# Kernel optimization log

Hardware: AMD Instinct MI355X
Metric: run time of the kernel (lower is better)

## Reference

```python
import jax, jax.numpy as jnp
import numpy as np
from jax import lax

SEQ, BATCH, IN, HID = 128, 512, 512, 512


def setup_inputs() -> dict:
    key = jax.random.key(0)
    k1, k2, k3 = jax.random.split(key, 3)
    # xavier_uniform over fan_in/fan_out of last two dims
    lim_ih = np.sqrt(6.0 / (IN + HID))
    lim_hh = np.sqrt(6.0 / (HID + HID))
    return {
        "inputs": jax.random.normal(k1, (SEQ, BATCH, IN), dtype=jnp.float32),
        "weight_ih": jax.random.uniform(k2, (8, IN, HID), jnp.float32, -lim_ih, lim_ih),
        "weight_hh": jax.random.uniform(k3, (8, HID, HID), jnp.float32, -lim_hh, lim_hh),
    }


def _cell(inp, state_c, state_m, weight_ih, weight_hh):
    # inp: [B, I]; states: [B, H]; weights: [8, I/H, H]
    s = jnp.einsum('bi,kih->kbh', inp, weight_ih) + jnp.einsum('bh,kho->kbo', state_m, weight_hh)
    l1_0 = jax.nn.sigmoid(s[0])
    l1_1 = jax.nn.relu(s[1])
    l1_2 = jax.nn.sigmoid(s[2])
    l1_3 = jax.nn.relu(s[3])
    l1_4 = jnp.tanh(s[4])
    l1_5 = jax.nn.sigmoid(s[5])
    l1_6 = jnp.tanh(s[6])
    l1_7 = jax.nn.sigmoid(s[7])
    l2_0 = jnp.tanh(l1_0 * l1_1)
    l2_1 = jnp.tanh(l1_2 + l1_3)
    l2_2 = jnp.tanh(l1_4 * l1_5)
    l2_3 = jax.nn.sigmoid(l1_6 + l1_7)
    l2_0_v2 = jnp.tanh(l2_0 + state_c)
    new_c = l2_0_v2 * l2_1
    l3_1 = jnp.tanh(l2_2 + l2_3)
    new_m = jnp.tanh(new_c * l3_1)
    return new_c, new_m


def reference(inputs, weight_ih, weight_hh):
    B = inputs.shape[1]
    H = weight_hh.shape[-1]
    init = (jnp.ones((B, H), inputs.dtype), jnp.ones((B, H), inputs.dtype))

    def step(carry, inp):
        c, m = carry
        c, m = _cell(inp, c, m, weight_ih, weight_hh)
        return (c, m), None

    (c, m), _ = lax.scan(step, init, inputs)
    return m
```

## Files before the change

### kernel.cpp

```cpp
#include <hip/hip_runtime.h>

#define SEQ  128
#define B_   512
#define IN_  512
#define HID_ 512
#define KTOT 1536
#define NTOT 4096
#define BM   64
#define BN   128
#define BK   64
#define NKT  (KTOT/BK)

typedef _Float16 f16;
typedef _Float16 f16x8 __attribute__((ext_vector_type(8)));
typedef _Float16 f16x4 __attribute__((ext_vector_type(4)));
typedef float    f32x4 __attribute__((ext_vector_type(4)));

#define OFF_BT  0u
#define OFF_X16 12582912u
#define OFF_C   79691776u
#define OFF_MH  80740352u
#define OFF_ML  81788928u

__device__ __forceinline__ void gll16(const void* g, void* l) {
  __builtin_amdgcn_global_load_lds(
      (const __attribute__((address_space(1))) unsigned int*)g,
      (__attribute__((address_space(3))) unsigned int*)l,
      16, 0, 0);
}

__device__ __forceinline__ float sigm_f(float x) {
  return __fdividef(1.f, 1.f + __expf(-x));
}
__device__ __forceinline__ float tanh_f(float x) {
  x = fminf(fmaxf(x, -15.f), 15.f);
  float u = __expf(2.f * x);
  return __fdividef(u - 1.f, u + 1.f);
}


__global__ void build_bt(const float* __restrict__ wih,
                         const float* __restrict__ whh,
                         f16* __restrict__ bt) {
  int n  = blockIdx.x;
  int hl = n & 15, k = (n >> 4) & 7, ht = n >> 7;
  int h  = ht * 16 + hl;
  const float* pih = wih + (size_t)k * IN_ * HID_ + h;
  const float* phh = whh + (size_t)k * HID_ * HID_ + h;
  f16* dst = bt + (size_t)n * KTOT;
  for (int r = threadIdx.x; r < 512; r += 256) {
    float a = pih[(size_t)r * HID_];
    float b = phh[(size_t)r * HID_];
    dst[r]        = (f16)a;
    dst[512 + r]  = (f16)b;
    dst[1024 + r] = (f16)b;
  }
}

__global__ void cvt_x(const float4* __restrict__ x, f16x4* __restrict__ y, int nvec) {
  int i = blockIdx.x * blockDim.x + threadIdx.x;
  int stride = gridDim.x * blockDim.x;
  for (; i < nvec; i += stride) {
    float4 v = x[i];
    f16x4 o = { (f16)v.x, (f16)v.y, (f16)v.z, (f16)v.w };
    y[i] = o;
  }
}

__global__ void init_state(float* __restrict__ c, f16* __restrict__ mh, f16* __restrict__ ml) {
  int i = blockIdx.x * blockDim.x + threadIdx.x;
  c[i]  = 1.f;
  mh[i] = (f16)1.f;
  ml[i] = (f16)0.f;
}

__global__ __launch_bounds__(256)
void nas_step(const f16* __restrict__ xt,
              const f16* __restrict__ bt,
              const f16* __restrict__ mh_in,
              const f16* __restrict__ ml_in,
              f16* __restrict__ mh_out,
              f16* __restrict__ ml_out,
              float* __restrict__ cst,
              float* __restrict__ out,
              int last) {
  __shared__ char lds[49152];
  char* Abase = lds;
  char* Bbase = lds + 16384;

  const int tid  = threadIdx.x;
  const int lane = tid & 63;
  const int wid  = tid >> 6;
  const int nt   = blockIdx.x;
  const int mt   = blockIdx.y;

  const f16* asrc[3] = { xt, mh_in, ml_in };

  auto stageA = [&](int buf, int kt) {
    const f16* src = asrc[kt >> 3];
    int kofs = (kt & 7) * BK;
#pragma unroll
    for (int p = 0; p < 2; ++p) {
      int u = p * 256 + tid;
      int r = u >> 3;
      int c16 = (u & 7) ^ (r & 7);
      gll16(src + ((size_t)(mt * BM + r) << 9) + kofs + c16 * 8,
            Abase + buf * 8192 + (p * 256 + wid * 64) * 16);
    }
  };
  auto stageB = [&](int buf, int kt) {
    int kg = kt * BK;
#pragma unroll
    for (int p = 0; p < 4; ++p) {
      int u = p * 256 + tid;
      int r = u >> 3;
      int c16 = (u & 7) ^ (r & 7);
      gll16(bt + (size_t)(nt * BN + r) * KTOT + kg + c16 * 8,
            Bbase + buf * 16384 + (p * 256 + wid * 64) * 16);
    }
  };

  f32x4 acc[8];
#pragma unroll
  for (int i = 0; i < 8; ++i) acc[i] = (f32x4){0.f, 0.f, 0.f, 0.f};

  stageA(0, 0); stageB(0, 0);
  __syncthreads();

  for (int kt = 0; kt < NKT; ++kt) {
    int cur = kt & 1;
    if (kt + 1 < NKT) { stageA(cur ^ 1, kt + 1); stageB(cur ^ 1, kt + 1); }
    const char* At = Abase + cur * 8192;
    const char* Bt = Bbase + cur * 16384;
#pragma unroll
    for (int kk = 0; kk < 2; ++kk) {
      int cb = (kk * 32 + ((lane >> 4) << 3)) * 2;
      int ra = wid * 16 + (lane & 15);
      f16x8 a = *(const f16x8*)(At + ra * 128 + (cb ^ ((ra & 7) << 4)));
#pragma unroll
      for (int ni = 0; ni < 8; ++ni) {
        int rb = ni * 16 + (lane & 15);
        f16x8 b = *(const f16x8*)(Bt + rb * 128 + (cb ^ ((rb & 7) << 4)));
        acc[ni] = __builtin_amdgcn_mfma_f32_16x16x32_f16(a, b, acc[ni], 0, 0, 0);
      }
    }
    __syncthreads();
  }

  const int h = nt * 16 + (lane & 15);
  const int rb4 = (lane >> 4) << 2;
#pragma unroll
  for (int q = 0; q < 4; ++q) {
    int b = mt * 64 + wid * 16 + rb4 + q;
    size_t idx = ((size_t)b << 9) + h;
    float l10 = sigm_f(acc[0][q]);
    float l11 = fmaxf(acc[1][q], 0.f);
    float l12 = sigm_f(acc[2][q]);
    float l13 = fmaxf(acc[3][q], 0.f);
    float l14 = tanh_f(acc[4][q]);
    float l15 = sigm_f(acc[5][q]);
    float l16 = tanh_f(acc[6][q]);
    float l17 = sigm_f(acc[7][q]);
    float l20 = tanh_f(l10 * l11);
    float l21 = tanh_f(l12 + l13);
    float l22 = tanh_f(l14 * l15);
    float l23 = sigm_f(l16 + l17);
    float cn  = tanh_f(l20 + cst[idx]) * l21;
    float l31 = tanh_f(l22 + l23);
    float mn  = tanh_f(cn * l31);
    cst[idx] = cn;
    f16 mh = (f16)mn;
    mh_out[idx] = mh;
    ml_out[idx] = (f16)(mn - (float)mh);
    if (last) out[idx] = mn;
  }
}

extern "C" void kernel_launch(void* const* d_in, const int* in_sizes, int n_in,
                              void* d_out, int out_size, void* d_ws, size_t ws_size,
                              hipStream_t stream) {
  const float* inputs = (const float*)d_in[0];
  const float* wih    = (const float*)d_in[1];
  const float* whh    = (const float*)d_in[2];
  float* out = (float*)d_out;
  char* ws   = (char*)d_ws;

  f16*   BT  = (f16*)(ws + OFF_BT);
  f16*   X16 = (f16*)(ws + OFF_X16);
  float* C   = (float*)(ws + OFF_C);
  f16*   MH  = (f16*)(ws + OFF_MH);
  f16*   ML  = (f16*)(ws + OFF_ML);

  build_bt<<<NTOT, 256, 0, stream>>>(wih, whh, BT);
  cvt_x<<<2048, 256, 0, stream>>>((const float4*)inputs, (f16x4*)X16,
                                  SEQ * B_ * IN_ / 4);
  init_state<<<1024, 256, 0, stream>>>(C, MH, ML);

  for (int t = 0; t < SEQ; ++t) {
    int cur = t & 1;
    nas_step<<<dim3(32, 8), 256, 0, stream>>>(
        X16 + (size_t)t * B_ * IN_, BT,
        MH + (size_t)cur * (B_ * HID_), ML + (size_t)cur * (B_ * HID_),
        MH + (size_t)(cur ^ 1) * (B_ * HID_), ML + (size_t)(cur ^ 1) * (B_ * HID_),
        C, out, (t == SEQ - 1) ? 1 : 0);
  }
}
```

Before: 2.234 ms.

## Fuse all timesteps into a persistent cooperative kernel with a grid barrier

Replaces the 128 per-timestep launches with one persistent cooperative kernel of 256 blocks. Blocks synchronise through an atomic counter in global memory and keep the cell state c in registers. A 5-slot LDS pipeline prefetches the next timestep's x tiles and the weight tiles across the barrier. The weight matrix is stored with a single copy of W_hh that serves both the m-high and m-low halves, and the B fragments are reused between them. This removes per-launch overhead and the global round-trips for c. In exchange it relies on all blocks being co-resident and on hand-tuned vmcnt waits, which could deadlock or race if the counts are wrong.

```diff
diff --git a/kernel.cpp b/kernel.cpp
--- a/kernel.cpp
+++ b/kernel.cpp
@@ -2,31 +2,27 @@
 
 #define SEQ  128
 #define B_   512
-#define IN_  512
 #define HID_ 512
-#define KTOT 1536
-#define NTOT 4096
-#define BM   64
-#define BN   128
-#define BK   64
-#define NKT  (KTOT/BK)
+#define NKT  24
 
 typedef _Float16 f16;
 typedef _Float16 f16x8 __attribute__((ext_vector_type(8)));
-typedef _Float16 f16x4 __attribute__((ext_vector_type(4)));
 typedef float    f32x4 __attribute__((ext_vector_type(4)));
 
-#define OFF_BT  0u
-#define OFF_X16 12582912u
-#define OFF_C   79691776u
-#define OFF_MH  80740352u
-#define OFF_ML  81788928u
+#define OFF_BT   0u
+#define OFF_X16  8388608u
+#define OFF_MH   75497472u
+#define OFF_ML   76546048u
+#define OFF_C    77594624u
+#define OFF_BAR  78643200u
+
+#define SLOT  24576
+#define NSLOT 5
 
 __device__ __forceinline__ void gll16(const void* g, void* l) {
   __builtin_amdgcn_global_load_lds(
       (const __attribute__((address_space(1))) unsigned int*)g,
-      (__attribute__((address_space(3))) unsigned int*)l,
-      16, 0, 0);
+      (__attribute__((address_space(3))) unsigned int*)l, 16, 0, 0);
 }
 
 __device__ __forceinline__ float sigm_f(float x) {
@@ -38,6 +34,7 @@
   return __fdividef(u - 1.f, u + 1.f);
 }
 
+#define VW(n) asm volatile("s_waitcnt vmcnt(" #n ")" ::: "memory")
 
 __global__ void build_bt(const float* __restrict__ wih,
                          const float* __restrict__ whh,
@@ -45,77 +42,225 @@
   int n  = blockIdx.x;
   int hl = n & 15, k = (n >> 4) & 7, ht = n >> 7;
   int h  = ht * 16 + hl;
-  const float* pih = wih + (size_t)k * IN_ * HID_ + h;
-  const float* phh = whh + (size_t)k * HID_ * HID_ + h;
-  f16* dst = bt + (size_t)n * KTOT;
+  const float* pih = wih + (size_t)k * 512 * 512 + h;
+  const float* phh = whh + (size_t)k * 512 * 512 + h;
+  f16* dst = bt + (size_t)n * 1024;
   for (int r = threadIdx.x; r < 512; r += 256) {
-    float a = pih[(size_t)r * HID_];
-    float b = phh[(size_t)r * HID_];
-    dst[r]        = (f16)a;
-    dst[512 + r]  = (f16)b;
-    dst[1024 + r] = (f16)b;
-  }
-}
-
-__global__ void cvt_x(const float4* __restrict__ x, f16x4* __restrict__ y, int nvec) {
+    dst[r]       = (f16)pih[(size_t)r * 512];
+    dst[512 + r] = (f16)phh[(size_t)r * 512];
+  }
+}
+
+__global__ void cvt_x(const float4* __restrict__ x, f16* __restrict__ y, int nvec) {
+  typedef _Float16 f16x4v __attribute__((ext_vector_type(4)));
   int i = blockIdx.x * blockDim.x + threadIdx.x;
   int stride = gridDim.x * blockDim.x;
+  f16x4v* yo = (f16x4v*)y;
   for (; i < nvec; i += stride) {
     float4 v = x[i];
-    f16x4 o = { (f16)v.x, (f16)v.y, (f16)v.z, (f16)v.w };
-    y[i] = o;
-  }
-}
-
-__global__ void init_state(float* __restrict__ c, f16* __restrict__ mh, f16* __restrict__ ml) {
+    f16x4v o = { (f16)v.x, (f16)v.y, (f16)v.z, (f16)v.w };
+    yo[i] = o;
+  }
+}
+
+__global__ void init_state(f16* __restrict__ mh, f16* __restrict__ ml,
+                           float* __restrict__ c, unsigned int* __restrict__ bar) {
   int i = blockIdx.x * blockDim.x + threadIdx.x;
-  c[i]  = 1.f;
   mh[i] = (f16)1.f;
   ml[i] = (f16)0.f;
+  c[i]  = 1.f;
+  if (i == 0) *bar = 0u;
+}
+
+__global__ __launch_bounds__(128, 1)
+void nas_persist(const f16* __restrict__ X, const f16* __restrict__ BT,
+                 f16* __restrict__ MHb, f16* __restrict__ MLb,
+                 unsigned int* __restrict__ bar, float* __restrict__ out) {
+  __shared__ char lds[NSLOT * SLOT];
+  const int tid  = threadIdx.x;
+  const int lane = tid & 63;
+  const int wid  = tid >> 6;
+  const int nt   = blockIdx.x & 31;
+  const int mt   = blockIdx.x >> 5;
+
+  auto stage = [&](int ti, int pi, int sl) {
+    const f16* asrc; int acol, bcol; bool hasb;
+    if (pi < 8) { asrc = X + (size_t)ti * 262144; acol = pi << 6; bcol = pi << 6; hasb = true; }
+    else {
+      int j = (pi - 8) >> 1;
+      asrc = ((pi & 1) ? MLb : MHb) + (size_t)(ti & 1) * 262144;
+      acol = j << 6; bcol = 512 + (j << 6); hasb = !(pi & 1);
+    }
+    char* As = lds + sl * SLOT;
+    char* Bs = As + 8192;
+#pragma unroll
+    for (int pp = 0; pp < 4; ++pp) {
+      int u = pp * 128 + tid; int r = u >> 3; int c = (u & 7) ^ (r & 7);
+      gll16(asrc + (((size_t)(mt * 64 + r)) << 9) + acol + c * 8,
+            As + (pp * 128 + wid * 64) * 16);
+    }
+    if (hasb) {
+#pragma unroll
+      for (int pp = 0; pp < 8; ++pp) {
+        int u = pp * 128 + tid; int r = u >> 3; int c = (u & 7) ^ (r & 7);
+        gll16(BT + (size_t)(nt * 128 + r) * 1024 + bcol + c * 8,
+              Bs + (pp * 128 + wid * 64) * 16);
+      }
+    }
+  };
+
+  f32x4 acc[2][8];
+  f16x8 bfr[2][8];
+  float creg[2][4];
+#pragma unroll
+  for (int mi = 0; mi < 2; ++mi)
+#pragma unroll
+    for (int q = 0; q < 4; ++q) creg[mi][q] = 1.f;
+
+  for (int pp = 0; pp < 4; ++pp) stage(0, pp, pp);
+
+  int s0 = 0;
+  for (int t = 0; t < SEQ; ++t) {
+#pragma unroll
+    for (int mi = 0; mi < 2; ++mi)
+#pragma unroll
+      for (int ni = 0; ni < 8; ++ni) acc[mi][ni] = (f32x4){0.f, 0.f, 0.f, 0.f};
+
+#pragma unroll
+    for (int p = 0; p < 24; ++p) {
+      if (p <= 5)       VW(36);
+      else if (p <= 7)  VW(28);
+      else if (p == 22) VW(28);
+      else if (p == 23) VW(36);
+      else if (p & 1)   VW(28);
+      else              VW(20);
+      __builtin_amdgcn_s_barrier();
+      asm volatile("" ::: "memory");
+
+      if (p == 4 && t > 0) {
+        if (tid == 0) {
+          while (__hip_atomic_load(bar, __ATOMIC_RELAXED, __HIP_MEMORY_SCOPE_AGENT)
+                 < (unsigned)(256 * t))
+            __builtin_amdgcn_s_sleep(2);
+          __builtin_amdgcn_fence(__ATOMIC_ACQUIRE, "agent");
+        }
+        __builtin_amdgcn_s_barrier();
+      }
+
+      {
+        int ti, pi;
+        if (p < 20) { ti = t; pi = p + 4; }
+        else        { ti = (t + 1 < SEQ) ? t + 1 : t; pi = p - 20; }
+        stage(ti, pi, (s0 + p + 4) % NSLOT);
+      }
+
+      {
+        const char* As = lds + ((s0 + p) % NSLOT) * SLOT;
+        const char* Bs = As + 8192;
+        const bool hasb = (p < 8) || !(p & 1);
+#pragma unroll
+        for (int kk = 0; kk < 2; ++kk) {
+          const int cb = (kk * 32 + ((lane >> 4) << 3)) * 2;
+          f16x8 a[2];
+#pragma unroll
+          for (int mi = 0; mi < 2; ++mi) {
+            int ra = wid * 32 + mi * 16 + (lane & 15);
+            a[mi] = *(const f16x8*)(As + ra * 128 + (cb ^ ((ra & 7) << 4)));
+          }
+          if (hasb) {
+#pragma unroll
+            for (int ni = 0; ni < 8; ++ni) {
+              int rb = ni * 16 + (lane & 15);
+              bfr[kk][ni] = *(const f16x8*)(Bs + rb * 128 + (cb ^ ((rb & 7) << 4)));
+            }
+          }
+#pragma unroll
+          for (int mi = 0; mi < 2; ++mi)
+#pragma unroll
+            for (int ni = 0; ni < 8; ++ni)
+              acc[mi][ni] = __builtin_amdgcn_mfma_f32_16x16x32_f16(
+                  a[mi], bfr[kk][ni], acc[mi][ni], 0, 0, 0);
+        }
+      }
+    }
+
+    {
+      const int h = nt * 16 + (lane & 15);
+      f16* mho = MHb + (size_t)((t & 1) ^ 1) * 262144;
+      f16* mlo = MLb + (size_t)((t & 1) ^ 1) * 262144;
+#pragma unroll
+      for (int mi = 0; mi < 2; ++mi) {
+#pragma unroll
+        for (int q = 0; q < 4; ++q) {
+          int b = mt * 64 + wid * 32 + mi * 16 + ((lane >> 4) << 2) + q;
+          size_t idx = ((size_t)b << 9) + h;
+          float l10 = sigm_f(acc[mi][0][q]);
+          float l11 = fmaxf(acc[mi][1][q], 0.f);
+          float l12 = sigm_f(acc[mi][2][q]);
+          float l13 = fmaxf(acc[mi][3][q], 0.f);
+          float l14 = tanh_f(acc[mi][4][q]);
+          float l15 = sigm_f(acc[mi][5][q]);
+          float l16 = tanh_f(acc[mi][6][q]);
+          float l17 = sigm_f(acc[mi][7][q]);
+          float l20 = tanh_f(l10 * l11);
+          float l21 = tanh_f(l12 + l13);
+          float l22 = tanh_f(l14 * l15);
+          float l23 = sigm_f(l16 + l17);
+          float cn  = tanh_f(l20 + creg[mi][q]) * l21;
+          float l31 = tanh_f(l22 + l23);
+          float mn  = tanh_f(cn * l31);
+          creg[mi][q] = cn;
+          f16 mhv = (f16)mn;
+          mho[idx] = mhv;
+          mlo[idx] = (f16)(mn - (float)mhv);
+          if (t == SEQ - 1) out[idx] = mn;
+        }
+      }
+    }
+
+    if (t < SEQ - 1) {
+      __builtin_amdgcn_fence(__ATOMIC_RELEASE, "agent");
+      __builtin_amdgcn_s_barrier();
+      if (tid == 0)
+        __hip_atomic_fetch_add(bar, 1u, __ATOMIC_RELAXED, __HIP_MEMORY_SCOPE_AGENT);
+    }
+
+    s0 += 4; if (s0 >= NSLOT) s0 -= NSLOT;
+  }
+  asm volatile("s_waitcnt vmcnt(0)" ::: "memory");
 }
 
 __global__ __launch_bounds__(256)
-void nas_step(const f16* __restrict__ xt,
-              const f16* __restrict__ bt,
-              const f16* __restrict__ mh_in,
-              const f16* __restrict__ ml_in,
-              f16* __restrict__ mh_out,
-              f16* __restrict__ ml_out,
-              float* __restrict__ cst,
-              float* __restrict__ out,
-              int last) {
+void nas_step(const f16* __restrict__ xt, const f16* __restrict__ bt,
+              const f16* __restrict__ mh_in, const f16* __restrict__ ml_in,
+              f16* __restrict__ mh_out, f16* __restrict__ ml_out,
+              float* __restrict__ cst, float* __restrict__ out, int last) {
   __shared__ char lds[49152];
   char* Abase = lds;
   char* Bbase = lds + 16384;
-
   const int tid  = threadIdx.x;
   const int lane = tid & 63;
   const int wid  = tid >> 6;
   const int nt   = blockIdx.x;
   const int mt   = blockIdx.y;
-
   const f16* asrc[3] = { xt, mh_in, ml_in };
 
   auto stageA = [&](int buf, int kt) {
     const f16* src = asrc[kt >> 3];
-    int kofs = (kt & 7) * BK;
+    int kofs = (kt & 7) * 64;
 #pragma unroll
     for (int p = 0; p < 2; ++p) {
-      int u = p * 256 + tid;
-      int r = u >> 3;
-      int c16 = (u & 7) ^ (r & 7);
-      gll16(src + ((size_t)(mt * BM + r) << 9) + kofs + c16 * 8,
+      int u = p * 256 + tid; int r = u >> 3; int c16 = (u & 7) ^ (r & 7);
+      gll16(src + ((size_t)(mt * 64 + r) << 9) + kofs + c16 * 8,
             Abase + buf * 8192 + (p * 256 + wid * 64) * 16);
     }
   };
   auto stageB = [&](int buf, int kt) {
-    int kg = kt * BK;
+    int kg = (kt < 8) ? (kt << 6) : (512 + ((kt & 7) << 6));
 #pragma unroll
     for (int p = 0; p < 4; ++p) {
-      int u = p * 256 + tid;
-      int r = u >> 3;
-      int c16 = (u & 7) ^ (r & 7);
-      gll16(bt + (size_t)(nt * BN + r) * KTOT + kg + c16 * 8,
+      int u = p * 256 + tid; int r = u >> 3; int c16 = (u & 7) ^ (r & 7);
+      gll16(bt + (size_t)(nt * 128 + r) * 1024 + kg + c16 * 8,
             Bbase + buf * 16384 + (p * 256 + wid * 64) * 16);
     }
   };
@@ -126,7 +271,6 @@
 
   stageA(0, 0); stageB(0, 0);
   __syncthreads();
-
   for (int kt = 0; kt < NKT; ++kt) {
     int cur = kt & 1;
     if (kt + 1 < NKT) { stageA(cur ^ 1, kt + 1); stageB(cur ^ 1, kt + 1); }
@@ -169,9 +313,9 @@
     float l31 = tanh_f(l22 + l23);
     float mn  = tanh_f(cn * l31);
     cst[idx] = cn;
-    f16 mh = (f16)mn;
-    mh_out[idx] = mh;
-    ml_out[idx] = (f16)(mn - (float)mh);
+    f16 mhv = (f16)mn;
+    mh_out[idx] = mhv;
+    ml_out[idx] = (f16)(mn - (float)mhv);
     if (last) out[idx] = mn;
   }
 }
@@ -185,23 +329,33 @@
   float* out = (float*)d_out;
   char* ws   = (char*)d_ws;
 
-  f16*   BT  = (f16*)(ws + OFF_BT);
-  f16*   X16 = (f16*)(ws + OFF_X16);
-  float* C   = (float*)(ws + OFF_C);
-  f16*   MH  = (f16*)(ws + OFF_MH);
-  f16*   ML  = (f16*)(ws + OFF_ML);
-
-  build_bt<<<NTOT, 256, 0, stream>>>(wih, whh, BT);
-  cvt_x<<<2048, 256, 0, stream>>>((const float4*)inputs, (f16x4*)X16,
-                                  SEQ * B_ * IN_ / 4);
-  init_state<<<1024, 256, 0, stream>>>(C, MH, ML);
-
-  for (int t = 0; t < SEQ; ++t) {
-    int cur = t & 1;
-    nas_step<<<dim3(32, 8), 256, 0, stream>>>(
-        X16 + (size_t)t * B_ * IN_, BT,
-        MH + (size_t)cur * (B_ * HID_), ML + (size_t)cur * (B_ * HID_),
-        MH + (size_t)(cur ^ 1) * (B_ * HID_), ML + (size_t)(cur ^ 1) * (B_ * HID_),
-        C, out, (t == SEQ - 1) ? 1 : 0);
-  }
-}
+  f16*          BTp = (f16*)(ws + OFF_BT);
+  f16*          Xp  = (f16*)(ws + OFF_X16);
+  f16*          MHp = (f16*)(ws + OFF_MH);
+  f16*          MLp = (f16*)(ws + OFF_ML);
+  float*        Cp  = (float*)(ws + OFF_C);
+  unsigned int* bp  = (unsigned int*)(ws + OFF_BAR);
+
+  build_bt<<<4096, 256, 0, stream>>>(wih, whh, BTp);
+  cvt_x<<<2048, 256, 0, stream>>>((const float4*)inputs, Xp, SEQ * B_ * 512 / 4);
+  init_state<<<1024, 256, 0, stream>>>(MHp, MLp, Cp, bp);
+
+  void* args[] = { (void*)&Xp, (void*)&BTp, (void*)&MHp, (void*)&MLp,
+                   (void*)&bp, (void*)&out };
+  hipError_t ce = hipLaunchCooperativeKernel((const void*)nas_persist, dim3(256),
+                                             dim3(128), args, 0, stream);
+  if (ce != hipSuccess) {
+    (void)hipGetLastError();
+    nas_persist<<<dim3(256), dim3(128), 0, stream>>>(Xp, BTp, MHp, MLp, bp, out);
+    if (hipGetLastError() != hipSuccess) {
+      for (int t = 0; t < SEQ; ++t) {
+        int cur = t & 1;
+        nas_step<<<dim3(32, 8), 256, 0, stream>>>(
+            Xp + (size_t)t * B_ * 512, BTp,
+            MHp + (size_t)cur * 262144, MLp + (size_t)cur * 262144,
+            MHp + (size_t)(cur ^ 1) * 262144, MLp + (size_t)(cur ^ 1) * 262144,
+            Cp, out, (t == SEQ - 1) ? 1 : 0);
+      }
+    }
+  }
+}
```

After: 3.609 ms. +61.5%, slower.
